# Optimization experiments

Hardware: AMD Instinct MI355X
Metric: run time of the kernel (lower is better)

## Reference

```python
import jax, jax.numpy as jnp
import numpy as np

N_NODES = 100000
N_EDGES = 3200000
N_GRAPHS = 64
IN_DIM, HID_DIM, EMB_DIM = 4, 64, 32


def setup_inputs() -> dict:
    key = jax.random.key(0)
    ks = jax.random.split(key, 9)
    x = jax.random.normal(ks[0], (N_NODES, IN_DIM), dtype=jnp.float32)
    edge_index = jax.random.randint(ks[1], (2, N_EDGES), 0, N_NODES, dtype=jnp.int32)
    batch = jnp.sort(jax.random.randint(ks[2], (N_NODES,), 0, N_GRAPHS, dtype=jnp.int32))
    def glorot(k, fan_in, fan_out):
        s = jnp.sqrt(6.0 / (fan_in + fan_out))
        return jax.random.uniform(k, (fan_in, fan_out), jnp.float32, -s, s)
    return {
        "x": x,
        "W1": glorot(ks[3], IN_DIM, HID_DIM), "b1": jnp.zeros((HID_DIM,), jnp.float32),
        "W2": glorot(ks[4], HID_DIM, HID_DIM), "b2": jnp.zeros((HID_DIM,), jnp.float32),
        "W3": glorot(ks[5], HID_DIM, EMB_DIM), "b3": jnp.zeros((EMB_DIM,), jnp.float32),
        "edge_index": edge_index,
        "batch": batch,
    }


def _gcn_conv(x, W, b, src, dst, dis):
    # PyG GCNConv: h = x W; out_i = sum_{j->i} (d_i d_j)^{-1/2} h_j  (self-loops included) + b
    h = x @ W                                   # [N, F_out]
    norm = dis[src] * dis[dst]                  # [E]
    agg = jax.ops.segment_sum(norm[:, None] * h[src], dst, num_segments=N_NODES)
    agg = agg + (dis * dis)[:, None] * h        # self-loop contribution (norm = d_i^{-1})
    return agg + b


def reference(x, W1, b1, W2, b2, W3, b3, edge_index, batch):
    src, dst = edge_index[0], edge_index[1]
    # degree with self-loops (counts in-edges at dst, matching PyG default flow)
    deg = jax.ops.segment_sum(jnp.ones_like(dst, dtype=jnp.float32), dst,
                              num_segments=N_NODES) + 1.0
    dis = jax.lax.rsqrt(deg)                    # deg_inv_sqrt, deg >= 1 always

    h = jax.nn.relu(_gcn_conv(x, W1, b1, src, dst, dis))
    h = jax.nn.relu(_gcn_conv(h, W2, b2, src, dst, dis))
    emb = _gcn_conv(h, W3, b3, src, dst, dis)   # [N, EMB_DIM]

    ones = jnp.ones((N_NODES,), jnp.float32)
    cnt = jax.ops.segment_sum(ones, batch, num_segments=N_GRAPHS)  # [G]
    feat_mean = jax.ops.segment_sum(emb, batch, num_segments=N_GRAPHS) / jnp.maximum(cnt, 1.0)[:, None]
    feat_max = jax.ops.segment_max(emb, batch, num_segments=N_GRAPHS)
    return jnp.concatenate([feat_mean, feat_max], axis=1)  # [G, 2*EMB_DIM]
```

## Files before the change

### kernel.cpp

```cpp
#include <hip/hip_runtime.h>
#include <hip/hip_bf16.h>

#define N_GRAPHS 64
#define TPAD 68


#define EBH 8192
__global__ void bucket_hist_kernel(const int* __restrict__ dst, int* __restrict__ bcnt,
                                   int E, int nbuck) {
    __shared__ int lh[512];
    const int tid = threadIdx.x;
    for (int i = tid; i < nbuck; i += 256) lh[i] = 0;
    __syncthreads();
    const int e0 = blockIdx.x * EBH;
    const int e1 = min(e0 + EBH, E);
    for (int e = e0 + tid; e < e1; e += 256)
        atomicAdd(&lh[((unsigned)dst[e]) >> 8], 1);
    __syncthreads();
    for (int i = tid; i < nbuck; i += 256) {
        int c = lh[i];
        if (c) atomicAdd(&bcnt[i], c);
    }
}

__global__ void bucket_scan_kernel(const int* __restrict__ bcnt, int* __restrict__ bbase,
                                   int* __restrict__ bcur, int nbuck) {
    __shared__ int sh[512];
    const int tid = threadIdx.x;
    int v = (tid < nbuck) ? bcnt[tid] : 0;
    sh[tid] = v;
    __syncthreads();
    for (int off = 1; off < 512; off <<= 1) {
        int t = (tid >= off) ? sh[tid - off] : 0;
        __syncthreads();
        sh[tid] += t;
        __syncthreads();
    }
    if (tid < nbuck) { int e = sh[tid] - v; bbase[tid] = e; bcur[tid] = e; }
    if (tid == nbuck - 1) bbase[nbuck] = sh[tid];
}


#define EBC 4096
__global__ void binscatter_kernel(const int* __restrict__ src, const int* __restrict__ dst,
                                  int* __restrict__ bcur, unsigned* __restrict__ binned,
                                  int E, int nbuck) {
    __shared__ int lhist[512];
    __shared__ int lbase[512];
    const int tid = threadIdx.x;
    const int e0 = blockIdx.x * EBC;
    const int e1 = min(e0 + EBC, E);
    for (int i = tid; i < nbuck; i += 256) lhist[i] = 0;
    __syncthreads();
    for (int e = e0 + tid; e < e1; e += 256) atomicAdd(&lhist[((unsigned)dst[e]) >> 8], 1);
    __syncthreads();
    for (int i = tid; i < nbuck; i += 256) {
        int c = lhist[i];
        lbase[i] = (c > 0) ? atomicAdd(&bcur[i], c) : 0;
        lhist[i] = 0;
    }
    __syncthreads();
    for (int e = e0 + tid; e < e1; e += 256) {
        int d = dst[e];
        int b = ((unsigned)d) >> 8;
        int off = atomicAdd(&lhist[b], 1);
        binned[lbase[b] + off] = ((unsigned)(d & 255) << 24) | (unsigned)src[e];
    }
}


__global__ void build_bucket_kernel(const unsigned* __restrict__ binned, const int* __restrict__ bbase,
                                    const float* __restrict__ x, int* __restrict__ rs,
                                    float* __restrict__ dis_g, float* __restrict__ Xs,
                                    int* __restrict__ col, int n) {
    __shared__ int cnt[256];
    __shared__ int lcur[256];
    __shared__ int wsum[4];
    const int b = blockIdx.x;
    const int node_base = b << 8;
    const int nb = min(256, n - node_base);
    const int tid = threadIdx.x;
    cnt[tid] = 0;
    __syncthreads();
    const int e0 = bbase[b], e1 = bbase[b + 1];
    for (int e = e0 + tid; e < e1; e += 256)
        atomicAdd(&cnt[binned[e] >> 24], 1);
    __syncthreads();
    const int deg = cnt[tid];
    const int lane = tid & 63, wid = tid >> 6;
    int s = deg;
    #pragma unroll
    for (int off = 1; off < 64; off <<= 1) {
        int t = __shfl_up(s, off);
        if (lane >= off) s += t;
    }
    if (lane == 63) wsum[wid] = s;
    __syncthreads();
    int woff = 0;
    for (int w = 0; w < wid; ++w) woff += wsum[w];
    const int excl = woff + s - deg;
    if (tid < nb) {
        int node = node_base + tid;
        rs[node] = e0 + excl;
        float d = rsqrtf((float)deg + 1.0f);
        dis_g[node] = d;
        float4 xv = *(const float4*)&x[node * 4];
        *(float4*)&Xs[node * 4] = make_float4(d * xv.x, d * xv.y, d * xv.z, d * xv.w);
    }
    lcur[tid] = e0 + excl;
    if (tid == 0 && node_base + nb == n) rs[n] = e1;
    __syncthreads();
    for (int e = e0 + tid; e < e1; e += 256) {
        unsigned v = binned[e];
        int p = atomicAdd(&lcur[v >> 24], 1);
        col[p] = (int)(v & 0xFFFFFFu);
    }
}


__global__ void agg4_kernel(const float* __restrict__ Xs, const int* __restrict__ col,
                            const int* __restrict__ rs, const float* __restrict__ dis,
                            float* __restrict__ aggX, int n) {
    int i = blockIdx.x * blockDim.x + threadIdx.x;
    if (i >= n) return;
    int e = rs[i];
    const int end = rs[i + 1];
    float4 a0 = make_float4(0, 0, 0, 0), a1 = make_float4(0, 0, 0, 0);
    for (; e + 2 <= end; e += 2) {
        int s0 = col[e], s1 = col[e + 1];
        float4 v0 = *(const float4*)&Xs[s0 * 4];
        float4 v1 = *(const float4*)&Xs[s1 * 4];
        a0.x += v0.x; a0.y += v0.y; a0.z += v0.z; a0.w += v0.w;
        a1.x += v1.x; a1.y += v1.y; a1.z += v1.z; a1.w += v1.w;
    }
    if (e < end) {
        float4 v = *(const float4*)&Xs[col[e] * 4];
        a0.x += v.x; a0.y += v.y; a0.z += v.z; a0.w += v.w;
    }
    float4 self = *(const float4*)&Xs[i * 4];
    float d = dis[i];
    float4 r = make_float4(d * (a0.x + a1.x + self.x), d * (a0.y + a1.y + self.y),
                           d * (a0.z + a1.z + self.z), d * (a0.w + a1.w + self.w));
    *(float4*)&aggX[i * 4] = r;
}

__global__ void transform1b_kernel(const float* __restrict__ aggX, const float* __restrict__ W1,
                                   const float* __restrict__ b1, float* __restrict__ H, int n) {
    int gid = blockIdx.x * blockDim.x + threadIdx.x;
    int i = gid >> 6, f = gid & 63;
    if (i >= n) return;
    float4 a = *(const float4*)&aggX[i * 4];
    float r = a.x * W1[f] + a.y * W1[64 + f] + a.z * W1[128 + f] + a.w * W1[192 + f] + b1[f];
    H[gid] = fmaxf(r, 0.0f);
}


__global__ void transform64_kernel(const float* __restrict__ h, const float* __restrict__ W,
                                   const float* __restrict__ dis, float* __restrict__ t, int n) {
    __shared__ float Wt[64 * TPAD];
    __shared__ float Hs[64 * TPAD];
    const int tid = threadIdx.x;
    const int base = blockIdx.x * 64;
    for (int idx = tid; idx < 4096; idx += 256) {
        int k = idx >> 6, f = idx & 63;
        Wt[f * TPAD + k] = W[idx];
    }
    for (int idx = tid; idx < 4096; idx += 256) {
        int nn = idx >> 6, k = idx & 63;
        int node = base + nn;
        Hs[nn * TPAD + k] = (node < n) ? h[node * 64 + k] : 0.0f;
    }
    __syncthreads();
    const int tf = tid & 15;
    const int tn = tid >> 4;
    float acc[4][4] = {};
    for (int k = 0; k < 64; k += 4) {
        float4 w4[4], h4[4];
        #pragma unroll
        for (int ff = 0; ff < 4; ++ff) w4[ff] = *(const float4*)&Wt[(tf * 4 + ff) * TPAD + k];
        #pragma unroll
        for (int nn = 0; nn < 4; ++nn) h4[nn] = *(const float4*)&Hs[(tn * 4 + nn) * TPAD + k];
        #pragma unroll
        for (int nn = 0; nn < 4; ++nn)
            #pragma unroll
            for (int ff = 0; ff < 4; ++ff)
                acc[nn][ff] += h4[nn].x * w4[ff].x + h4[nn].y * w4[ff].y +
                               h4[nn].z * w4[ff].z + h4[nn].w * w4[ff].w;
    }
    #pragma unroll
    for (int nn = 0; nn < 4; ++nn) {
        int node = base + tn * 4 + nn;
        if (node < n) {
            float d = dis[node];
            float4 o = make_float4(d * acc[nn][0], d * acc[nn][1], d * acc[nn][2], d * acc[nn][3]);
            *(float4*)&t[node * 64 + tf * 4] = o;
        }
    }
}

__global__ void transform64_32_kernel(const float* __restrict__ h, const float* __restrict__ W,
                                      const float* __restrict__ dis, float* __restrict__ t, int n) {
    __shared__ float Wt[32 * TPAD];
    __shared__ float Hs[128 * TPAD];
    const int tid = threadIdx.x;
    const int base = blockIdx.x * 128;
    for (int idx = tid; idx < 2048; idx += 256) {
        int k = idx >> 5, f = idx & 31;
        Wt[f * TPAD + k] = W[idx];
    }
    for (int idx = tid; idx < 8192; idx += 256) {
        int nn = idx >> 6, k = idx & 63;
        int node = base + nn;
        Hs[nn * TPAD + k] = (node < n) ? h[node * 64 + k] : 0.0f;
    }
    __syncthreads();
    const int tf = tid & 7;
    const int tn = tid >> 3;
    float acc[4][4] = {};
    for (int k = 0; k < 64; k += 4) {
        float4 w4[4], h4[4];
        #pragma unroll
        for (int ff = 0; ff < 4; ++ff) w4[ff] = *(const float4*)&Wt[(tf * 4 + ff) * TPAD + k];
        #pragma unroll
        for (int nn = 0; nn < 4; ++nn) h4[nn] = *(const float4*)&Hs[(tn * 4 + nn) * TPAD + k];
        #pragma unroll
        for (int nn = 0; nn < 4; ++nn)
            #pragma unroll
            for (int ff = 0; ff < 4; ++ff)
                acc[nn][ff] += h4[nn].x * w4[ff].x + h4[nn].y * w4[ff].y +
                               h4[nn].z * w4[ff].z + h4[nn].w * w4[ff].w;
    }
    #pragma unroll
    for (int nn = 0; nn < 4; ++nn) {
        int node = base + tn * 4 + nn;
        if (node < n) {
            float d = dis[node];
            float4 o = make_float4(d * acc[nn][0], d * acc[nn][1], d * acc[nn][2], d * acc[nn][3]);
            *(float4*)&t[node * 32 + tf * 4] = o;
        }
    }
}


template <int F, bool RELU>
__global__ void aggregate_kernel(const float* __restrict__ t, const int* __restrict__ col,
                                 const int* __restrict__ rs, const float* __restrict__ dis,
                                 const float* __restrict__ b, float* __restrict__ out, int n) {
    int gid = blockIdx.x * blockDim.x + threadIdx.x;
    int i, f;
    if (F == 64) { i = gid >> 6; f = threadIdx.x & 63; }
    else         { i = gid >> 5; f = threadIdx.x & 31; }
    if (i >= n) return;
    float acc0 = 0.0f, acc1 = 0.0f;
    int e = rs[i];
    const int end = rs[i + 1];
    for (; e + 8 <= end; e += 8) {
        int s0 = col[e],     s1 = col[e + 1], s2 = col[e + 2], s3 = col[e + 3];
        int s4 = col[e + 4], s5 = col[e + 5], s6 = col[e + 6], s7 = col[e + 7];
        float v0 = t[s0 * F + f], v1 = t[s1 * F + f], v2 = t[s2 * F + f], v3 = t[s3 * F + f];
        float v4 = t[s4 * F + f], v5 = t[s5 * F + f], v6 = t[s6 * F + f], v7 = t[s7 * F + f];
        acc0 += v0; acc1 += v1; acc0 += v2; acc1 += v3;
        acc0 += v4; acc1 += v5; acc0 += v6; acc1 += v7;
    }
    for (; e < end; ++e) acc0 += t[col[e] * F + f];
    float r = dis[i] * (acc0 + acc1 + t[i * F + f]) + b[f];
    if (RELU) r = fmaxf(r, 0.0f);
    out[i * F + f] = r;
}


__device__ __forceinline__ unsigned mapf(float v) {
    unsigned u = __float_as_uint(v);
    return u ^ ((u & 0x80000000u) ? 0xFFFFFFFFu : 0x80000000u);
}

#define MAPPED_NEG_INF 0x007FFFFFu

__global__ void init_readout_kernel(float* __restrict__ gsum, unsigned* __restrict__ gmax,
                                    int* __restrict__ gcnt) {
    int idx = blockIdx.x * blockDim.x + threadIdx.x;
    if (idx < N_GRAPHS * 32) { gsum[idx] = 0.0f; gmax[idx] = MAPPED_NEG_INF; }
    if (idx < N_GRAPHS) gcnt[idx] = 0;
}

#define R_CHUNK 512
__global__ void readout_kernel(const float* __restrict__ emb, const int* __restrict__ batch,
                               float* __restrict__ gsum, unsigned* __restrict__ gmax,
                               int* __restrict__ gcnt, int n) {
    __shared__ float ssum[N_GRAPHS * 32];
    __shared__ unsigned smax[N_GRAPHS * 32];
    __shared__ int scnt[N_GRAPHS];
    const int tid = threadIdx.x;
    for (int idx = tid; idx < N_GRAPHS * 32; idx += 256) { ssum[idx] = 0.0f; smax[idx] = MAPPED_NEG_INF; }
    if (tid < N_GRAPHS) scnt[tid] = 0;
    __syncthreads();
    const int lane = tid & 31, grp = tid >> 5;
    const int start = blockIdx.x * R_CHUNK;
    const int end = min(start + R_CHUNK, n);
    for (int i = start + grp; i < end; i += 8) {
        int g = batch[i];
        float v = emb[i * 32 + lane];
        atomicAdd(&ssum[g * 32 + lane], v);
        atomicMax(&smax[g * 32 + lane], mapf(v));
        if (lane == 0) atomicAdd(&scnt[g], 1);
    }
    __syncthreads();
    for (int idx = tid; idx < N_GRAPHS * 32; idx += 256) {
        int g = idx >> 5;
        if (scnt[g] > 0) {
            atomicAdd(&gsum[idx], ssum[idx]);
            atomicMax(&gmax[idx], smax[idx]);
        }
    }
    if (tid < N_GRAPHS && scnt[tid] > 0) atomicAdd(&gcnt[tid], scnt[tid]);
}

__global__ void finalize_kernel(const float* __restrict__ gsum, const unsigned* __restrict__ gmax,
                                const int* __restrict__ gcnt, float* __restrict__ out) {
    int idx = blockIdx.x * blockDim.x + threadIdx.x;
    if (idx >= N_GRAPHS * 32) return;
    int g = idx >> 5, f = idx & 31;
    float c = fmaxf((float)gcnt[g], 1.0f);
    out[g * 64 + f] = gsum[idx] / c;
    unsigned u = gmax[idx];
    unsigned bits = (u & 0x80000000u) ? (u ^ 0x80000000u) : ~u;
    out[g * 64 + 32 + f] = __uint_as_float(bits);
}


extern "C" void kernel_launch(void* const* d_in, const int* in_sizes, int n_in,
                              void* d_out, int out_size, void* d_ws, size_t ws_size,
                              hipStream_t stream) {
    const float* x  = (const float*)d_in[0];
    const float* W1 = (const float*)d_in[1];
    const float* b1 = (const float*)d_in[2];
    const float* W2 = (const float*)d_in[3];
    const float* b2 = (const float*)d_in[4];
    const float* W3 = (const float*)d_in[5];
    const float* b3 = (const float*)d_in[6];
    const int* edge_index = (const int*)d_in[7];
    const int* batch = (const int*)d_in[8];
    float* out = (float*)d_out;

    const int N = in_sizes[0] / 4;
    const int E = in_sizes[7] / 2;
    const int* src = edge_index;
    const int* dst = edge_index + E;
    const int nbuck = (N + 255) >> 8;

    char* p = (char*)d_ws;
    auto alloc = [&](size_t bytes) { void* r = (void*)p; p += (bytes + 255) & ~(size_t)255; return r; };
    int*      rs   = (int*)alloc((size_t)(N + 1) * 4);
    float*    dis  = (float*)alloc((size_t)N * 4);
    int*      col  = (int*)alloc((size_t)E * 4);
    float*    T    = (float*)alloc((size_t)N * 64 * 4);
    float*    H    = (float*)alloc((size_t)N * 64 * 4);
    int*      bcnt = (int*)alloc((size_t)512 * 4);
    int*      bbase= (int*)alloc((size_t)513 * 4);
    int*      bcur = (int*)alloc((size_t)512 * 4);
    float*    gsum = (float*)alloc((size_t)N_GRAPHS * 32 * 4);
    unsigned* gmax = (unsigned*)alloc((size_t)N_GRAPHS * 32 * 4);
    int*      gcnt = (int*)alloc((size_t)N_GRAPHS * 4);
    unsigned* binned = (unsigned*)T;
    float*    Xs     = T + (size_t)E;
    float*    aggX   = T + (size_t)E + (size_t)N * 4;
    (void)ws_size; (void)n_in; (void)out_size;

    const int gN = (N + 255) / 256;

    hipMemsetAsync(bcnt, 0, 512 * 4, stream);
    bucket_hist_kernel<<<(E + EBH - 1) / EBH, 256, 0, stream>>>(dst, bcnt, E, nbuck);
    bucket_scan_kernel<<<1, 512, 0, stream>>>(bcnt, bbase, bcur, nbuck);
    binscatter_kernel<<<(E + EBC - 1) / EBC, 256, 0, stream>>>(src, dst, bcur, binned, E, nbuck);
    build_bucket_kernel<<<nbuck, 256, 0, stream>>>(binned, bbase, x, rs, dis, Xs, col, N);

    agg4_kernel<<<gN, 256, 0, stream>>>(Xs, col, rs, dis, aggX, N);
    transform1b_kernel<<<(N * 64 + 255) / 256, 256, 0, stream>>>(aggX, W1, b1, H, N);
    transform64_kernel<<<(N + 63) / 64, 256, 0, stream>>>(H, W2, dis, T, N);
    aggregate_kernel<64, true><<<(N * 64 + 255) / 256, 256, 0, stream>>>(T, col, rs, dis, b2, H, N);
    transform64_32_kernel<<<(N + 127) / 128, 256, 0, stream>>>(H, W3, dis, T, N);
    aggregate_kernel<32, false><<<(N * 32 + 255) / 256, 256, 0, stream>>>(T, col, rs, dis, b3, H, N);

    init_readout_kernel<<<(N_GRAPHS * 32 + 255) / 256, 256, 0, stream>>>(gsum, gmax, gcnt);
    readout_kernel<<<(N + R_CHUNK - 1) / R_CHUNK, 256, 0, stream>>>(H, batch, gsum, gmax, gcnt, N);
    finalize_kernel<<<(N_GRAPHS * 32 + 255) / 256, 256, 0, stream>>>(gsum, gmax, gcnt, out);
}
```

Measured before the change: 402.0 us.

## Fuse GCN transforms into aggregation kernels and sort CSR columns by source tile

The layer-1 bias/ReLU is folded into the W2 transform, and the 64-wide aggregation is fused with the W3 projection, so neither the H buffer nor a separate transform pass is needed. The CSR build now counting-sorts each node's neighbours into 16 source-index tiles, which should make gathers more cache-local. Costs are a larger shared-memory histogram in the build kernel and a 4-node-per-block aggregation with a serial 64-term dot product per output that may lower occupancy or efficiency.

Result: faster. 378.5 us (-5.8%).

```diff
diff --git a/kernel.cpp b/kernel.cpp
--- a/kernel.cpp
+++ b/kernel.cpp
@@ -3,6 +3,8 @@
 
 #define N_GRAPHS 64
 #define TPAD 68
+#define NT 16
+#define TSHIFT 13
 
 
 #define EBH 8192
@@ -73,20 +75,26 @@
                                     const float* __restrict__ x, int* __restrict__ rs,
                                     float* __restrict__ dis_g, float* __restrict__ Xs,
                                     int* __restrict__ col, int n) {
-    __shared__ int cnt[256];
-    __shared__ int lcur[256];
+    __shared__ int cnt2[256 * NT];
     __shared__ int wsum[4];
     const int b = blockIdx.x;
     const int node_base = b << 8;
     const int nb = min(256, n - node_base);
     const int tid = threadIdx.x;
-    cnt[tid] = 0;
+    #pragma unroll
+    for (int t = 0; t < NT; ++t) cnt2[tid * NT + t] = 0;
     __syncthreads();
     const int e0 = bbase[b], e1 = bbase[b + 1];
-    for (int e = e0 + tid; e < e1; e += 256)
-        atomicAdd(&cnt[binned[e] >> 24], 1);
-    __syncthreads();
-    const int deg = cnt[tid];
+    for (int e = e0 + tid; e < e1; e += 256) {
+        unsigned v = binned[e];
+        int dloc = v >> 24;
+        int t = (int)((v & 0xFFFFFFu) >> TSHIFT);
+        atomicAdd(&cnt2[dloc * NT + t], 1);
+    }
+    __syncthreads();
+    int deg = 0;
+    #pragma unroll
+    for (int t = 0; t < NT; ++t) deg += cnt2[tid * NT + t];
     const int lane = tid & 63, wid = tid >> 6;
     int s = deg;
     #pragma unroll
@@ -99,6 +107,13 @@
     int woff = 0;
     for (int w = 0; w < wid; ++w) woff += wsum[w];
     const int excl = woff + s - deg;
+    int run = e0 + excl;
+    #pragma unroll
+    for (int t = 0; t < NT; ++t) {
+        int c = cnt2[tid * NT + t];
+        cnt2[tid * NT + t] = run;
+        run += c;
+    }
     if (tid < nb) {
         int node = node_base + tid;
         rs[node] = e0 + excl;
@@ -107,13 +122,15 @@
         float4 xv = *(const float4*)&x[node * 4];
         *(float4*)&Xs[node * 4] = make_float4(d * xv.x, d * xv.y, d * xv.z, d * xv.w);
     }
-    lcur[tid] = e0 + excl;
     if (tid == 0 && node_base + nb == n) rs[n] = e1;
     __syncthreads();
     for (int e = e0 + tid; e < e1; e += 256) {
         unsigned v = binned[e];
-        int p = atomicAdd(&lcur[v >> 24], 1);
-        col[p] = (int)(v & 0xFFFFFFu);
+        int dloc = v >> 24;
+        int srcv = (int)(v & 0xFFFFFFu);
+        int t = srcv >> TSHIFT;
+        int p = atomicAdd(&cnt2[dloc * NT + t], 1);
+        col[p] = srcv;
     }
 }
 
@@ -144,31 +161,33 @@
     *(float4*)&aggX[i * 4] = r;
 }
 
-__global__ void transform1b_kernel(const float* __restrict__ aggX, const float* __restrict__ W1,
-                                   const float* __restrict__ b1, float* __restrict__ H, int n) {
-    int gid = blockIdx.x * blockDim.x + threadIdx.x;
-    int i = gid >> 6, f = gid & 63;
-    if (i >= n) return;
-    float4 a = *(const float4*)&aggX[i * 4];
-    float r = a.x * W1[f] + a.y * W1[64 + f] + a.z * W1[128 + f] + a.w * W1[192 + f] + b1[f];
-    H[gid] = fmaxf(r, 0.0f);
-}
-
-
-__global__ void transform64_kernel(const float* __restrict__ h, const float* __restrict__ W,
-                                   const float* __restrict__ dis, float* __restrict__ t, int n) {
+
+__global__ void fused_l1_kernel(const float* __restrict__ aggX, const float* __restrict__ W1,
+                                const float* __restrict__ b1, const float* __restrict__ W2,
+                                const float* __restrict__ dis, float* __restrict__ t, int n) {
+    __shared__ float W1s[256];
+    __shared__ float b1s[64];
     __shared__ float Wt[64 * TPAD];
     __shared__ float Hs[64 * TPAD];
     const int tid = threadIdx.x;
     const int base = blockIdx.x * 64;
+    if (tid < 256) W1s[tid] = W1[tid];
+    if (tid < 64) b1s[tid] = b1[tid];
     for (int idx = tid; idx < 4096; idx += 256) {
         int k = idx >> 6, f = idx & 63;
-        Wt[f * TPAD + k] = W[idx];
-    }
+        Wt[f * TPAD + k] = W2[idx];
+    }
+    __syncthreads();
     for (int idx = tid; idx < 4096; idx += 256) {
         int nn = idx >> 6, k = idx & 63;
         int node = base + nn;
-        Hs[nn * TPAD + k] = (node < n) ? h[node * 64 + k] : 0.0f;
+        float v = 0.0f;
+        if (node < n) {
+            float4 a = *(const float4*)&aggX[node * 4];
+            v = fmaxf(a.x * W1s[k] + a.y * W1s[64 + k] + a.z * W1s[128 + k] + a.w * W1s[192 + k]
+                      + b1s[k], 0.0f);
+        }
+        Hs[nn * TPAD + k] = v;
     }
     __syncthreads();
     const int tf = tid & 15;
@@ -198,58 +217,56 @@
     }
 }
 
-__global__ void transform64_32_kernel(const float* __restrict__ h, const float* __restrict__ W,
-                                      const float* __restrict__ dis, float* __restrict__ t, int n) {
-    __shared__ float Wt[32 * TPAD];
-    __shared__ float Hs[128 * TPAD];
-    const int tid = threadIdx.x;
-    const int base = blockIdx.x * 128;
-    for (int idx = tid; idx < 2048; idx += 256) {
-        int k = idx >> 5, f = idx & 31;
-        Wt[f * TPAD + k] = W[idx];
-    }
-    for (int idx = tid; idx < 8192; idx += 256) {
-        int nn = idx >> 6, k = idx & 63;
-        int node = base + nn;
-        Hs[nn * TPAD + k] = (node < n) ? h[node * 64 + k] : 0.0f;
-    }
-    __syncthreads();
-    const int tf = tid & 7;
-    const int tn = tid >> 3;
-    float acc[4][4] = {};
-    for (int k = 0; k < 64; k += 4) {
-        float4 w4[4], h4[4];
-        #pragma unroll
-        for (int ff = 0; ff < 4; ++ff) w4[ff] = *(const float4*)&Wt[(tf * 4 + ff) * TPAD + k];
-        #pragma unroll
-        for (int nn = 0; nn < 4; ++nn) h4[nn] = *(const float4*)&Hs[(tn * 4 + nn) * TPAD + k];
-        #pragma unroll
-        for (int nn = 0; nn < 4; ++nn)
+
+__global__ void agg64_fused_kernel(const float* __restrict__ t, const int* __restrict__ col,
+                                   const int* __restrict__ rs, const float* __restrict__ dis,
+                                   const float* __restrict__ b2, const float* __restrict__ W3,
+                                   float* __restrict__ t32, int n) {
+    __shared__ float W3s[2048];
+    __shared__ float rrow[4 * 65];
+    __shared__ float disl[4];
+    const int tid = threadIdx.x;
+    for (int idx = tid; idx < 2048; idx += 256) W3s[idx] = W3[idx];
+    const int w = tid >> 6, f = tid & 63;
+    const int i = blockIdx.x * 4 + w;
+    if (i < n) {
+        float acc0 = 0.0f, acc1 = 0.0f;
+        int e = rs[i];
+        const int end = rs[i + 1];
+        for (; e + 8 <= end; e += 8) {
+            int s0 = col[e],     s1 = col[e + 1], s2 = col[e + 2], s3 = col[e + 3];
+            int s4 = col[e + 4], s5 = col[e + 5], s6 = col[e + 6], s7 = col[e + 7];
+            float v0 = t[s0 * 64 + f], v1 = t[s1 * 64 + f], v2 = t[s2 * 64 + f], v3 = t[s3 * 64 + f];
+            float v4 = t[s4 * 64 + f], v5 = t[s5 * 64 + f], v6 = t[s6 * 64 + f], v7 = t[s7 * 64 + f];
+            acc0 += v0; acc1 += v1; acc0 += v2; acc1 += v3;
+            acc0 += v4; acc1 += v5; acc0 += v6; acc1 += v7;
+        }
+        for (; e < end; ++e) acc0 += t[col[e] * 64 + f];
+        float di = dis[i];
+        float r = fmaxf(di * (acc0 + acc1 + t[i * 64 + f]) + b2[f], 0.0f);
+        rrow[w * 65 + f] = r;
+        if (f == 0) disl[w] = di;
+    }
+    __syncthreads();
+    if (tid < 128) {
+        int q = tid >> 5, c = tid & 31;
+        int node = blockIdx.x * 4 + q;
+        if (node < n) {
+            float dot = 0.0f;
             #pragma unroll
-            for (int ff = 0; ff < 4; ++ff)
-                acc[nn][ff] += h4[nn].x * w4[ff].x + h4[nn].y * w4[ff].y +
-                               h4[nn].z * w4[ff].z + h4[nn].w * w4[ff].w;
-    }
-    #pragma unroll
-    for (int nn = 0; nn < 4; ++nn) {
-        int node = base + tn * 4 + nn;
-        if (node < n) {
-            float d = dis[node];
-            float4 o = make_float4(d * acc[nn][0], d * acc[nn][1], d * acc[nn][2], d * acc[nn][3]);
-            *(float4*)&t[node * 32 + tf * 4] = o;
+            for (int ff = 0; ff < 64; ++ff)
+                dot += rrow[q * 65 + ff] * W3s[ff * 32 + c];
+            t32[node * 32 + c] = disl[q] * dot;
         }
     }
 }
 
 
-template <int F, bool RELU>
-__global__ void aggregate_kernel(const float* __restrict__ t, const int* __restrict__ col,
-                                 const int* __restrict__ rs, const float* __restrict__ dis,
-                                 const float* __restrict__ b, float* __restrict__ out, int n) {
+__global__ void agg32_kernel(const float* __restrict__ t, const int* __restrict__ col,
+                             const int* __restrict__ rs, const float* __restrict__ dis,
+                             const float* __restrict__ b, float* __restrict__ out, int n) {
     int gid = blockIdx.x * blockDim.x + threadIdx.x;
-    int i, f;
-    if (F == 64) { i = gid >> 6; f = threadIdx.x & 63; }
-    else         { i = gid >> 5; f = threadIdx.x & 31; }
+    int i = gid >> 5, f = threadIdx.x & 31;
     if (i >= n) return;
     float acc0 = 0.0f, acc1 = 0.0f;
     int e = rs[i];
@@ -257,15 +274,13 @@
     for (; e + 8 <= end; e += 8) {
         int s0 = col[e],     s1 = col[e + 1], s2 = col[e + 2], s3 = col[e + 3];
         int s4 = col[e + 4], s5 = col[e + 5], s6 = col[e + 6], s7 = col[e + 7];
-        float v0 = t[s0 * F + f], v1 = t[s1 * F + f], v2 = t[s2 * F + f], v3 = t[s3 * F + f];
-        float v4 = t[s4 * F + f], v5 = t[s5 * F + f], v6 = t[s6 * F + f], v7 = t[s7 * F + f];
+        float v0 = t[s0 * 32 + f], v1 = t[s1 * 32 + f], v2 = t[s2 * 32 + f], v3 = t[s3 * 32 + f];
+        float v4 = t[s4 * 32 + f], v5 = t[s5 * 32 + f], v6 = t[s6 * 32 + f], v7 = t[s7 * 32 + f];
         acc0 += v0; acc1 += v1; acc0 += v2; acc1 += v3;
         acc0 += v4; acc1 += v5; acc0 += v6; acc1 += v7;
     }
-    for (; e < end; ++e) acc0 += t[col[e] * F + f];
-    float r = dis[i] * (acc0 + acc1 + t[i * F + f]) + b[f];
-    if (RELU) r = fmaxf(r, 0.0f);
-    out[i * F + f] = r;
+    for (; e < end; ++e) acc0 += t[col[e] * 32 + f];
+    out[i * 32 + f] = dis[i] * (acc0 + acc1 + t[i * 32 + f]) + b[f];
 }
 
 
@@ -353,8 +368,10 @@
     int*      rs   = (int*)alloc((size_t)(N + 1) * 4);
     float*    dis  = (float*)alloc((size_t)N * 4);
     int*      col  = (int*)alloc((size_t)E * 4);
+    float*    Xs   = (float*)alloc((size_t)N * 4 * 4);
+    float*    aggX = (float*)alloc((size_t)N * 4 * 4);
     float*    T    = (float*)alloc((size_t)N * 64 * 4);
-    float*    H    = (float*)alloc((size_t)N * 64 * 4);
+    float*    T32  = (float*)alloc((size_t)N * 32 * 4);
     int*      bcnt = (int*)alloc((size_t)512 * 4);
     int*      bbase= (int*)alloc((size_t)513 * 4);
     int*      bcur = (int*)alloc((size_t)512 * 4);
@@ -362,8 +379,7 @@
     unsigned* gmax = (unsigned*)alloc((size_t)N_GRAPHS * 32 * 4);
     int*      gcnt = (int*)alloc((size_t)N_GRAPHS * 4);
     unsigned* binned = (unsigned*)T;
-    float*    Xs     = T + (size_t)E;
-    float*    aggX   = T + (size_t)E + (size_t)N * 4;
+    float*    H32    = T;
     (void)ws_size; (void)n_in; (void)out_size;
 
     const int gN = (N + 255) / 256;
@@ -375,13 +391,11 @@
     build_bucket_kernel<<<nbuck, 256, 0, stream>>>(binned, bbase, x, rs, dis, Xs, col, N);
 
     agg4_kernel<<<gN, 256, 0, stream>>>(Xs, col, rs, dis, aggX, N);
-    transform1b_kernel<<<(N * 64 + 255) / 256, 256, 0, stream>>>(aggX, W1, b1, H, N);
-    transform64_kernel<<<(N + 63) / 64, 256, 0, stream>>>(H, W2, dis, T, N);
-    aggregate_kernel<64, true><<<(N * 64 + 255) / 256, 256, 0, stream>>>(T, col, rs, dis, b2, H, N);
-    transform64_32_kernel<<<(N + 127) / 128, 256, 0, stream>>>(H, W3, dis, T, N);
-    aggregate_kernel<32, false><<<(N * 32 + 255) / 256, 256, 0, stream>>>(T, col, rs, dis, b3, H, N);
+    fused_l1_kernel<<<(N + 63) / 64, 256, 0, stream>>>(aggX, W1, b1, W2, dis, T, N);
+    agg64_fused_kernel<<<(N + 3) / 4, 256, 0, stream>>>(T, col, rs, dis, b2, W3, T32, N);
+    agg32_kernel<<<(N * 32 + 255) / 256, 256, 0, stream>>>(T32, col, rs, dis, b3, H32, N);
 
     init_readout_kernel<<<(N_GRAPHS * 32 + 255) / 256, 256, 0, stream>>>(gsum, gmax, gcnt);
-    readout_kernel<<<(N + R_CHUNK - 1) / R_CHUNK, 256, 0, stream>>>(H, batch, gsum, gmax, gcnt, N);
+    readout_kernel<<<(N + R_CHUNK - 1) / R_CHUNK, 256, 0, stream>>>(H32, batch, gsum, gmax, gcnt, N);
     finalize_kernel<<<(N_GRAPHS * 32 + 255) / 256, 256, 0, stream>>>(gsum, gmax, gcnt, out);
 }
```

## Sort edges by source tile per wave group for streaming cache-local aggregation

Applied to the files above, without the earlier changes.

The edge binning now groups destinations into buckets of 200 nodes. Within each bucket, edges are sub-sorted by (wave group of 25 nodes, source tile of 8192 nodes, node), with per-tile counts stored as bytes. A new wave-per-25-nodes aggregation kernel sweeps the source tiles in order, so gathered feature rows stay in a cache-sized window. Separately, the layer-1 transform with ReLU is fused into the 64x64 transform kernel. The cost is that each wave walks its edges serially with little memory-level parallelism, only about 4000 waves are launched, and lanes are idle or duplicated for F=4 and F=32.

Result: slower. 1.268 ms (+215.5%).

```diff
diff --git a/kernel.cpp b/kernel.cpp
--- a/kernel.cpp
+++ b/kernel.cpp
@@ -3,6 +3,13 @@
 
 #define N_GRAPHS 64
 #define TPAD 68
+#define NT 16
+#define TSHIFT 13
+#define NBW2 200
+#define WPB 8
+#define NPW 25
+#define NKEY 3200
+#define NKEYP 3328
 
 
 #define EBH 8192
@@ -10,12 +17,12 @@
                                    int E, int nbuck) {
     __shared__ int lh[512];
     const int tid = threadIdx.x;
-    for (int i = tid; i < nbuck; i += 256) lh[i] = 0;
+    for (int i = tid; i < 512; i += 256) lh[i] = 0;
     __syncthreads();
     const int e0 = blockIdx.x * EBH;
     const int e1 = min(e0 + EBH, E);
     for (int e = e0 + tid; e < e1; e += 256)
-        atomicAdd(&lh[((unsigned)dst[e]) >> 8], 1);
+        atomicAdd(&lh[dst[e] / NBW2], 1);
     __syncthreads();
     for (int i = tid; i < nbuck; i += 256) {
         int c = lh[i];
@@ -50,9 +57,9 @@
     const int tid = threadIdx.x;
     const int e0 = blockIdx.x * EBC;
     const int e1 = min(e0 + EBC, E);
-    for (int i = tid; i < nbuck; i += 256) lhist[i] = 0;
-    __syncthreads();
-    for (int e = e0 + tid; e < e1; e += 256) atomicAdd(&lhist[((unsigned)dst[e]) >> 8], 1);
+    for (int i = tid; i < 512; i += 256) lhist[i] = 0;
+    __syncthreads();
+    for (int e = e0 + tid; e < e1; e += 256) atomicAdd(&lhist[dst[e] / NBW2], 1);
     __syncthreads();
     for (int i = tid; i < nbuck; i += 256) {
         int c = lhist[i];
@@ -62,33 +69,54 @@
     __syncthreads();
     for (int e = e0 + tid; e < e1; e += 256) {
         int d = dst[e];
-        int b = ((unsigned)d) >> 8;
+        int b = d / NBW2;
         int off = atomicAdd(&lhist[b], 1);
-        binned[lbase[b] + off] = ((unsigned)(d & 255) << 24) | (unsigned)src[e];
-    }
-}
-
-
-__global__ void build_bucket_kernel(const unsigned* __restrict__ binned, const int* __restrict__ bbase,
-                                    const float* __restrict__ x, int* __restrict__ rs,
-                                    float* __restrict__ dis_g, float* __restrict__ Xs,
-                                    int* __restrict__ col, int n) {
-    __shared__ int cnt[256];
-    __shared__ int lcur[256];
+        binned[lbase[b] + off] = ((unsigned)(d - b * NBW2) << 24) | (unsigned)src[e];
+    }
+}
+
+
+__global__ void build_stream_kernel(const unsigned* __restrict__ binned, const int* __restrict__ bbase,
+                                    const float* __restrict__ x, float* __restrict__ dis_g,
+                                    float* __restrict__ Xs, int* __restrict__ col3,
+                                    unsigned char* __restrict__ cnt8, int* __restrict__ wstart,
+                                    int n) {
+    __shared__ int ck[NKEYP];
     __shared__ int wsum[4];
     const int b = blockIdx.x;
-    const int node_base = b << 8;
-    const int nb = min(256, n - node_base);
-    const int tid = threadIdx.x;
-    cnt[tid] = 0;
+    const int node_base = b * NBW2;
+    const int tid = threadIdx.x;
+    for (int i = tid; i < NKEYP; i += 256) ck[i] = 0;
     __syncthreads();
     const int e0 = bbase[b], e1 = bbase[b + 1];
-    for (int e = e0 + tid; e < e1; e += 256)
-        atomicAdd(&cnt[binned[e] >> 24], 1);
-    __syncthreads();
-    const int deg = cnt[tid];
+    for (int e = e0 + tid; e < e1; e += 256) {
+        unsigned v = binned[e];
+        int dloc = v >> 24;
+        int t = (int)((v & 0xFFFFFFu) >> TSHIFT);
+        atomicAdd(&ck[(dloc / NPW) * 400 + t * 25 + (dloc % NPW)], 1);
+    }
+    __syncthreads();
+    if (tid < NBW2) {
+        int node = node_base + tid;
+        if (node < n) {
+            int wl = tid / NPW, k = tid % NPW;
+            int deg = 0;
+            #pragma unroll
+            for (int t = 0; t < NT; ++t) deg += ck[wl * 400 + t * 25 + k];
+            float d = rsqrtf((float)deg + 1.0f);
+            dis_g[node] = d;
+            float4 xv = *(const float4*)&x[node * 4];
+            *(float4*)&Xs[node * 4] = make_float4(d * xv.x, d * xv.y, d * xv.z, d * xv.w);
+        }
+    }
+    for (int i = tid; i < NKEY; i += 256) cnt8[(size_t)b * NKEY + i] = (unsigned char)ck[i];
+    __syncthreads();
+    const int base_i = tid * 13;
+    int lsum = 0;
+    #pragma unroll
+    for (int j = 0; j < 13; ++j) lsum += ck[base_i + j];
     const int lane = tid & 63, wid = tid >> 6;
-    int s = deg;
+    int s = lsum;
     #pragma unroll
     for (int off = 1; off < 64; off <<= 1) {
         int t = __shfl_up(s, off);
@@ -98,77 +126,92 @@
     __syncthreads();
     int woff = 0;
     for (int w = 0; w < wid; ++w) woff += wsum[w];
-    const int excl = woff + s - deg;
-    if (tid < nb) {
-        int node = node_base + tid;
-        rs[node] = e0 + excl;
-        float d = rsqrtf((float)deg + 1.0f);
-        dis_g[node] = d;
-        float4 xv = *(const float4*)&x[node * 4];
-        *(float4*)&Xs[node * 4] = make_float4(d * xv.x, d * xv.y, d * xv.z, d * xv.w);
-    }
-    lcur[tid] = e0 + excl;
-    if (tid == 0 && node_base + nb == n) rs[n] = e1;
+    int run = e0 + woff + s - lsum;
+    #pragma unroll
+    for (int j = 0; j < 13; ++j) { int c = ck[base_i + j]; ck[base_i + j] = run; run += c; }
+    __syncthreads();
+    if (tid < WPB) wstart[b * WPB + tid] = ck[tid * 400];
     __syncthreads();
     for (int e = e0 + tid; e < e1; e += 256) {
         unsigned v = binned[e];
-        int p = atomicAdd(&lcur[v >> 24], 1);
-        col[p] = (int)(v & 0xFFFFFFu);
-    }
-}
-
-
-__global__ void agg4_kernel(const float* __restrict__ Xs, const int* __restrict__ col,
-                            const int* __restrict__ rs, const float* __restrict__ dis,
-                            float* __restrict__ aggX, int n) {
-    int i = blockIdx.x * blockDim.x + threadIdx.x;
-    if (i >= n) return;
-    int e = rs[i];
-    const int end = rs[i + 1];
-    float4 a0 = make_float4(0, 0, 0, 0), a1 = make_float4(0, 0, 0, 0);
-    for (; e + 2 <= end; e += 2) {
-        int s0 = col[e], s1 = col[e + 1];
-        float4 v0 = *(const float4*)&Xs[s0 * 4];
-        float4 v1 = *(const float4*)&Xs[s1 * 4];
-        a0.x += v0.x; a0.y += v0.y; a0.z += v0.z; a0.w += v0.w;
-        a1.x += v1.x; a1.y += v1.y; a1.z += v1.z; a1.w += v1.w;
-    }
-    if (e < end) {
-        float4 v = *(const float4*)&Xs[col[e] * 4];
-        a0.x += v.x; a0.y += v.y; a0.z += v.z; a0.w += v.w;
-    }
-    float4 self = *(const float4*)&Xs[i * 4];
-    float d = dis[i];
-    float4 r = make_float4(d * (a0.x + a1.x + self.x), d * (a0.y + a1.y + self.y),
-                           d * (a0.z + a1.z + self.z), d * (a0.w + a1.w + self.w));
-    *(float4*)&aggX[i * 4] = r;
-}
-
-__global__ void transform1b_kernel(const float* __restrict__ aggX, const float* __restrict__ W1,
-                                   const float* __restrict__ b1, float* __restrict__ H, int n) {
-    int gid = blockIdx.x * blockDim.x + threadIdx.x;
-    int i = gid >> 6, f = gid & 63;
-    if (i >= n) return;
-    float4 a = *(const float4*)&aggX[i * 4];
-    float r = a.x * W1[f] + a.y * W1[64 + f] + a.z * W1[128 + f] + a.w * W1[192 + f] + b1[f];
-    H[gid] = fmaxf(r, 0.0f);
-}
-
-
-__global__ void transform64_kernel(const float* __restrict__ h, const float* __restrict__ W,
-                                   const float* __restrict__ dis, float* __restrict__ t, int n) {
+        int dloc = v >> 24;
+        int srcv = (int)(v & 0xFFFFFFu);
+        int t = srcv >> TSHIFT;
+        int p = atomicAdd(&ck[(dloc / NPW) * 400 + t * 25 + (dloc % NPW)], 1);
+        col3[p] = srcv;
+    }
+}
+
+
+template <int F, bool RELU, bool BIAS>
+__global__ __launch_bounds__(256, 4)
+void agg_stream_kernel(const float* __restrict__ t, const int* __restrict__ col3,
+                       const unsigned char* __restrict__ cnt8, const int* __restrict__ wstart,
+                       const float* __restrict__ dis, const float* __restrict__ bias,
+                       float* __restrict__ out, int n, int nwave) {
+    const int tid = threadIdx.x;
+    const int w = blockIdx.x * 4 + (tid >> 6);
+    if (w >= nwave) return;
+    const int lane = tid & 63;
+    const int fl = lane & (F - 1);
+    float acc[NPW];
+    #pragma unroll
+    for (int k = 0; k < NPW; ++k) acc[k] = 0.0f;
+    int cur = wstart[w];
+    const size_t cbase = (size_t)w * 400;
+    for (int tp = 0; tp < NT; ++tp) {
+        int cntv = (lane < NPW) ? (int)cnt8[cbase + tp * 25 + lane] : 0;
+        #pragma unroll
+        for (int k = 0; k < NPW; ++k) {
+            const int c = __shfl(cntv, k);
+            for (int j = 0; j < c; ++j) {
+                int s = col3[cur + j];
+                acc[k] += t[(size_t)s * F + fl];
+            }
+            cur += c;
+        }
+    }
+    const int nodeb = w * NPW;
+    const float bv = BIAS ? bias[fl] : 0.0f;
+    #pragma unroll
+    for (int k = 0; k < NPW; ++k) {
+        int i = nodeb + k;
+        if (i < n && lane < F) {
+            float d = dis[i];
+            float r = d * (acc[k] + t[(size_t)i * F + fl]) + bv;
+            if (RELU) r = fmaxf(r, 0.0f);
+            out[(size_t)i * F + fl] = r;
+        }
+    }
+}
+
+
+__global__ void fused_l1_kernel(const float* __restrict__ aggX, const float* __restrict__ W1,
+                                const float* __restrict__ b1, const float* __restrict__ W2,
+                                const float* __restrict__ dis, float* __restrict__ t, int n) {
+    __shared__ float W1s[256];
+    __shared__ float b1s[64];
     __shared__ float Wt[64 * TPAD];
     __shared__ float Hs[64 * TPAD];
     const int tid = threadIdx.x;
     const int base = blockIdx.x * 64;
+    if (tid < 256) W1s[tid] = W1[tid];
+    if (tid < 64) b1s[tid] = b1[tid];
     for (int idx = tid; idx < 4096; idx += 256) {
         int k = idx >> 6, f = idx & 63;
-        Wt[f * TPAD + k] = W[idx];
-    }
+        Wt[f * TPAD + k] = W2[idx];
+    }
+    __syncthreads();
     for (int idx = tid; idx < 4096; idx += 256) {
         int nn = idx >> 6, k = idx & 63;
         int node = base + nn;
-        Hs[nn * TPAD + k] = (node < n) ? h[node * 64 + k] : 0.0f;
+        float v = 0.0f;
+        if (node < n) {
+            float4 a = *(const float4*)&aggX[node * 4];
+            v = fmaxf(a.x * W1s[k] + a.y * W1s[64 + k] + a.z * W1s[128 + k] + a.w * W1s[192 + k]
+                      + b1s[k], 0.0f);
+        }
+        Hs[nn * TPAD + k] = v;
     }
     __syncthreads();
     const int tf = tid & 15;
@@ -198,6 +241,7 @@
     }
 }
 
+
 __global__ void transform64_32_kernel(const float* __restrict__ h, const float* __restrict__ W,
                                       const float* __restrict__ dis, float* __restrict__ t, int n) {
     __shared__ float Wt[32 * TPAD];
@@ -239,33 +283,6 @@
             *(float4*)&t[node * 32 + tf * 4] = o;
         }
     }
-}
-
-
-template <int F, bool RELU>
-__global__ void aggregate_kernel(const float* __restrict__ t, const int* __restrict__ col,
-                                 const int* __restrict__ rs, const float* __restrict__ dis,
-                                 const float* __restrict__ b, float* __restrict__ out, int n) {
-    int gid = blockIdx.x * blockDim.x + threadIdx.x;
-    int i, f;
-    if (F == 64) { i = gid >> 6; f = threadIdx.x & 63; }
-    else         { i = gid >> 5; f = threadIdx.x & 31; }
-    if (i >= n) return;
-    float acc0 = 0.0f, acc1 = 0.0f;
-    int e = rs[i];
-    const int end = rs[i + 1];
-    for (; e + 8 <= end; e += 8) {
-        int s0 = col[e],     s1 = col[e + 1], s2 = col[e + 2], s3 = col[e + 3];
-        int s4 = col[e + 4], s5 = col[e + 5], s6 = col[e + 6], s7 = col[e + 7];
-        float v0 = t[s0 * F + f], v1 = t[s1 * F + f], v2 = t[s2 * F + f], v3 = t[s3 * F + f];
-        float v4 = t[s4 * F + f], v5 = t[s5 * F + f], v6 = t[s6 * F + f], v7 = t[s7 * F + f];
-        acc0 += v0; acc1 += v1; acc0 += v2; acc1 += v3;
-        acc0 += v4; acc1 += v5; acc0 += v6; acc1 += v7;
-    }
-    for (; e < end; ++e) acc0 += t[col[e] * F + f];
-    float r = dis[i] * (acc0 + acc1 + t[i * F + f]) + b[f];
-    if (RELU) r = fmaxf(r, 0.0f);
-    out[i * F + f] = r;
 }
 
 
@@ -346,42 +363,44 @@
     const int E = in_sizes[7] / 2;
     const int* src = edge_index;
     const int* dst = edge_index + E;
-    const int nbuck = (N + 255) >> 8;
+    const int nbuck = (N + NBW2 - 1) / NBW2;
+    const int nwave = nbuck * WPB;
+    const int gstream = (nwave + 3) / 4;
 
     char* p = (char*)d_ws;
     auto alloc = [&](size_t bytes) { void* r = (void*)p; p += (bytes + 255) & ~(size_t)255; return r; };
-    int*      rs   = (int*)alloc((size_t)(N + 1) * 4);
-    float*    dis  = (float*)alloc((size_t)N * 4);
-    int*      col  = (int*)alloc((size_t)E * 4);
-    float*    T    = (float*)alloc((size_t)N * 64 * 4);
-    float*    H    = (float*)alloc((size_t)N * 64 * 4);
-    int*      bcnt = (int*)alloc((size_t)512 * 4);
-    int*      bbase= (int*)alloc((size_t)513 * 4);
-    int*      bcur = (int*)alloc((size_t)512 * 4);
-    float*    gsum = (float*)alloc((size_t)N_GRAPHS * 32 * 4);
-    unsigned* gmax = (unsigned*)alloc((size_t)N_GRAPHS * 32 * 4);
-    int*      gcnt = (int*)alloc((size_t)N_GRAPHS * 4);
+    float*         dis    = (float*)alloc((size_t)N * 4);
+    int*           col3   = (int*)alloc((size_t)E * 4);
+    unsigned char* cnt8   = (unsigned char*)alloc((size_t)nbuck * NKEY);
+    int*           wstart = (int*)alloc((size_t)nwave * 4);
+    float*         T      = (float*)alloc((size_t)N * 64 * 4);
+    float*         H      = (float*)alloc((size_t)N * 64 * 4);
+    int*           bcnt   = (int*)alloc((size_t)512 * 4);
+    int*           bbase  = (int*)alloc((size_t)513 * 4);
+    int*           bcur   = (int*)alloc((size_t)512 * 4);
+    float*         gsum   = (float*)alloc((size_t)N_GRAPHS * 32 * 4);
+    unsigned*      gmax   = (unsigned*)alloc((size_t)N_GRAPHS * 32 * 4);
+    int*           gcnt   = (int*)alloc((size_t)N_GRAPHS * 4);
     unsigned* binned = (unsigned*)T;
-    float*    Xs     = T + (size_t)E;
-    float*    aggX   = T + (size_t)E + (size_t)N * 4;
+    float*    Xs     = H;
+    float*    aggX   = H + (size_t)N * 4;
+    float*    T32    = T;
+    float*    H32    = H;
     (void)ws_size; (void)n_in; (void)out_size;
-
-    const int gN = (N + 255) / 256;
 
     hipMemsetAsync(bcnt, 0, 512 * 4, stream);
     bucket_hist_kernel<<<(E + EBH - 1) / EBH, 256, 0, stream>>>(dst, bcnt, E, nbuck);
     bucket_scan_kernel<<<1, 512, 0, stream>>>(bcnt, bbase, bcur, nbuck);
     binscatter_kernel<<<(E + EBC - 1) / EBC, 256, 0, stream>>>(src, dst, bcur, binned, E, nbuck);
-    build_bucket_kernel<<<nbuck, 256, 0, stream>>>(binned, bbase, x, rs, dis, Xs, col, N);
-
-    agg4_kernel<<<gN, 256, 0, stream>>>(Xs, col, rs, dis, aggX, N);
-    transform1b_kernel<<<(N * 64 + 255) / 256, 256, 0, stream>>>(aggX, W1, b1, H, N);
-    transform64_kernel<<<(N + 63) / 64, 256, 0, stream>>>(H, W2, dis, T, N);
-    aggregate_kernel<64, true><<<(N * 64 + 255) / 256, 256, 0, stream>>>(T, col, rs, dis, b2, H, N);
-    transform64_32_kernel<<<(N + 127) / 128, 256, 0, stream>>>(H, W3, dis, T, N);
-    aggregate_kernel<32, false><<<(N * 32 + 255) / 256, 256, 0, stream>>>(T, col, rs, dis, b3, H, N);
+    build_stream_kernel<<<nbuck, 256, 0, stream>>>(binned, bbase, x, dis, Xs, col3, cnt8, wstart, N);
+
+    agg_stream_kernel<4, false, false><<<gstream, 256, 0, stream>>>(Xs, col3, cnt8, wstart, dis, b1, aggX, N, nwave);
+    fused_l1_kernel<<<(N + 63) / 64, 256, 0, stream>>>(aggX, W1, b1, W2, dis, T, N);
+    agg_stream_kernel<64, true, true><<<gstream, 256, 0, stream>>>(T, col3, cnt8, wstart, dis, b2, H, N, nwave);
+    transform64_32_kernel<<<(N + 127) / 128, 256, 0, stream>>>(H, W3, dis, T32, N);
+    agg_stream_kernel<32, false, true><<<gstream, 256, 0, stream>>>(T32, col3, cnt8, wstart, dis, b3, H32, N, nwave);
 
     init_readout_kernel<<<(N_GRAPHS * 32 + 255) / 256, 256, 0, stream>>>(gsum, gmax, gcnt);
-    readout_kernel<<<(N + R_CHUNK - 1) / R_CHUNK, 256, 0, stream>>>(H, batch, gsum, gmax, gcnt, N);
+    readout_kernel<<<(N + R_CHUNK - 1) / R_CHUNK, 256, 0, stream>>>(H32, batch, gsum, gmax, gcnt, N);
     finalize_kernel<<<(N_GRAPHS * 32 + 255) / 256, 256, 0, stream>>>(gsum, gmax, gcnt, out);
 }
```
